# Performance work log

Hardware: AMD Instinct MI355X
Metric: run time of the kernel (lower is better)

The kernel has to match this reference:

```python
import jax, jax.numpy as jnp
import numpy as np
from functools import partial

BN_EPS = 1e-5

def conv2d(x, w, pad):
    # x: [N,C,H,W], w: [O,I,kh,kw]
    return jax.lax.conv_general_dilated(
        x, w, window_strides=(1, 1), padding=((pad, pad), (pad, pad)),
        dimension_numbers=("NCHW", "OIHW", "NCHW"))

def bn_prelu(x, gamma, beta, mean, var, alpha):
    # eval-mode BatchNorm2d followed by single-parameter PReLU
    scale = gamma * jax.lax.rsqrt(var + BN_EPS)
    h = x * scale[None, :, None, None] + (beta - mean * scale)[None, :, None, None]
    return jnp.where(h >= 0, h, alpha * h)

def unfold3x3(x):
    # torch nn.Unfold(3, padding=1): output layout [N, C*9, H*W]
    N, C, H, W = x.shape
    xp = jnp.pad(x, ((0, 0), (0, 0), (1, 1), (1, 1)))
    patches = jnp.stack(
        [xp[:, :, i:i + H, j:j + W] for i in range(3) for j in range(3)],
        axis=2)  # [N, C, 9, H, W] -- row-major identical to [N, C*9, H*W]
    return patches

def setup_inputs() -> dict:
    key = jax.random.key(0)
    ks = jax.random.split(key, 16)
    N, C, H, W = 16, 256, 64, 64
    K2 = 9
    inp = {
        "x": jax.random.normal(ks[0], (N, C, H, W), jnp.float32),
        "y": jax.random.normal(ks[1], (N, C, H, W), jnp.float32),
        # gernerate_kernel_spatial[0]: Conv3x3 C->C + BN + PReLU
        "W1": jax.random.normal(ks[2], (C, C, 3, 3), jnp.float32) * 0.05,
        "g1": jax.random.normal(ks[3], (C,), jnp.float32) * 0.1 + 1.0,
        "b1": jax.random.normal(ks[4], (C,), jnp.float32) * 0.1,
        "m1": jax.random.normal(ks[5], (C,), jnp.float32) * 0.1,
        "v1": jax.random.uniform(ks[6], (C,), jnp.float32, 0.5, 1.5),
        "a1": jnp.float32(0.25),
        # gernerate_kernel_spatial[1]: Conv1x1 C->9 + BN + PReLU
        "W2": jax.random.normal(ks[7], (K2, C, 1, 1), jnp.float32) * 0.05,
        "g2": jax.random.normal(ks[8], (K2,), jnp.float32) * 0.1 + 1.0,
        "b2": jax.random.normal(ks[9], (K2,), jnp.float32) * 0.1,
        "m2": jax.random.normal(ks[10], (K2,), jnp.float32) * 0.1,
        "v2": jax.random.uniform(ks[11], (K2,), jnp.float32, 0.5, 1.5),
        "a2": jnp.float32(0.25),
    }
    return inp

def reference(x, y, W1, g1, b1, m1, v1, a1, W2, g2, b2, m2, v2, a2):
    N, C, H, W = x.shape
    # dynamic per-pixel 3x3 kernel from y: [N, 9, H, W]
    h = bn_prelu(conv2d(y, W1, pad=1), g1, b1, m1, v1, a1)
    kernel = bn_prelu(conv2d(h, W2, pad=0), g2, b2, m2, v2, a2)
    # kernel.reshape(N,9,H,W,1).permute(0,2,3,1,4) -> [N,H,W,9]
    kern = jnp.transpose(kernel, (0, 2, 3, 1))
    # unfold(x) is [N, C*9, H*W]; torch reshapes it ROW-MAJOR to [N,H,W,C,9]
    ux = unfold3x3(x).reshape(N, H, W, C, 9)
    # matmul [N,H,W,C,9] @ [N,H,W,9,1] -> squeeze -> permute to NCHW
    out = jnp.einsum("nhwck,nhwk->nchw", ux, kern)
    return out
```

## Files before the change

kernel.cpp:

```cpp
#include <hip/hip_runtime.h>
#include <hip/hip_bf16.h>

typedef __attribute__((ext_vector_type(8))) short bf16x8;
typedef __attribute__((ext_vector_type(4))) float f32x4;
typedef __attribute__((ext_vector_type(8))) unsigned short u16x8;
typedef __attribute__((ext_vector_type(4))) unsigned short u16x4;

#define BN_EPS 1e-5f

__device__ __forceinline__ unsigned short f2bf(float f) {
  unsigned int u = __float_as_uint(f);
  unsigned int r = u + 0x7FFFu + ((u >> 16) & 1u);
  return (unsigned short)(r >> 16);
}
__device__ __forceinline__ float bf2f(unsigned short u) {
  union { float f; unsigned int i; } v; v.i = ((unsigned int)u) << 16; return v.f;
}

__device__ __forceinline__ void async_ld16(const unsigned short* g, unsigned short* l) {
  __builtin_amdgcn_global_load_lds(
      (const __attribute__((address_space(1))) void*)g,
      (__attribute__((address_space(3))) void*)l, 16, 0, 0);
}

__global__ __launch_bounds__(256) void fold_w1_kernel(
    const float* __restrict__ W1, const float* __restrict__ g1,
    const float* __restrict__ b1, const float* __restrict__ m1,
    const float* __restrict__ v1, const float* __restrict__ W2,
    const float* __restrict__ g2, const float* __restrict__ b2,
    const float* __restrict__ m2, const float* __restrict__ v2,
    unsigned short* __restrict__ Bt, float* __restrict__ bias1,
    float* __restrict__ W2f, float* __restrict__ bias2)
{
  int o = blockIdx.x;
  int t = threadIdx.x;
  if (o == 0) {
    float s1 = g1[t] * rsqrtf(v1[t] + BN_EPS);
    bias1[t] = b1[t] - m1[t] * s1;
    for (int i = t; i < 2304; i += 256) {
      int j = i >> 8;
      float s2 = g2[j] * rsqrtf(v2[j] + BN_EPS);
      W2f[i] = W2[i] * s2;
    }
    if (t < 9) {
      float s2 = g2[t] * rsqrtf(v2[t] + BN_EPS);
      bias2[t] = b2[t] - m2[t] * s2;
    }
  }
  float s = g1[o] * rsqrtf(v1[o] + BN_EPS);
  const float* src = W1 + (size_t)o * 2304 + (size_t)t * 9;
  int chunk = t >> 5, q = (t >> 3) & 3, e = t & 7;
  #pragma unroll
  for (int tap = 0; tap < 9; ++tap) {
    float wv = src[tap] * s;
    int ct = chunk * 9 + tap;
    Bt[(((size_t)ct * 4 + q) * 256 + o) * 8 + e] = f2bf(wv);
  }
}

__global__ __launch_bounds__(256) void transpose_pad_kernel(
    const float* __restrict__ y, unsigned short* __restrict__ yTp)
{
  __shared__ unsigned short T[64][68];
  int t = threadIdx.x;
  int nb = blockIdx.x; int n = nb >> 6, h = nb & 63;
  int w4 = (t & 15) * 4;
  int cl = t >> 4;
  for (int cb = 0; cb < 4; ++cb) {
    __syncthreads();
    #pragma unroll
    for (int r = 0; r < 4; ++r) {
      int c = cb * 64 + cl + r * 16;
      float4 v = *(const float4*)(y + ((((size_t)n * 256 + c) * 64 + h) << 6) + w4);
      u16x4 pv = { f2bf(v.x), f2bf(v.y), f2bf(v.z), f2bf(v.w) };
      *(u16x4*)&T[cl + r * 16][w4] = pv;
    }
    __syncthreads();
    size_t base = ((((size_t)n * 32 + cb * 8) * 66 + (h + 1)) * 66 + 1) * 8;
    #pragma unroll
    for (int pass = 0; pass < 2; ++pass) {
      int w = pass * 32 + (t >> 3);
      int c8 = t & 7;
      u16x8 o;
      #pragma unroll
      for (int i = 0; i < 8; ++i) o[i] = T[c8 * 8 + i][w];
      *(u16x8*)(yTp + base + ((size_t)c8 * (66 * 66) + w) * 8) = o;
    }
  }
  u16x8 z = (u16x8){0, 0, 0, 0, 0, 0, 0, 0};
  size_t nb32 = (size_t)n * 32;
  if (t < 64) {
    int qg = t & 31, side = t >> 5;
    *(u16x8*)(yTp + (((nb32 + qg) * 66 + (h + 1)) * 66 + side * 65) * 8) = z;
  }
  if (h == 0) {
    for (int i = t; i < 2112; i += 256) {
      int qg = i / 66, ww = i - qg * 66;
      *(u16x8*)(yTp + (((nb32 + qg) * 66 + 0) * 66 + ww) * 8) = z;
      *(u16x8*)(yTp + (((nb32 + qg) * 66 + 65) * 66 + ww) * 8) = z;
    }
  }
}

__global__ __launch_bounds__(256, 2) void conv3x3_mfma_kernel(
    const unsigned short* __restrict__ yTp, const unsigned short* __restrict__ Bt,
    const float* __restrict__ bias1, const float* __restrict__ a1p,
    const float* __restrict__ W2f, const float* __restrict__ bias2,
    const float* __restrict__ a2p, float* __restrict__ kernP)
{
  __shared__ union SM {
    struct { unsigned short A[2][4][4][66][8];
             unsigned short B[2][4][256][8]; } m;
    unsigned short h[128][264];
  } sm;
  __shared__ float w2s[2304];

  int tid = threadIdx.x;
  int w = tid >> 6, l = tid & 63;
  int lr = l & 15, quad = l >> 4;
  int wm = w >> 1, wn = w & 1;
  int bm = blockIdx.x;
  int n = bm >> 5, hb = (bm & 31) * 2;

  for (int i = tid; i < 2304; i += 256) w2s[i] = W2f[i];

  f32x4 acc[4][8];
  #pragma unroll
  for (int im = 0; im < 4; ++im)
    #pragma unroll
    for (int in_ = 0; in_ < 8; ++in_)
      acc[im][in_] = (f32x4){0.f, 0.f, 0.f, 0.f};

  const unsigned short* gaP =
      yTp + (((size_t)n * 32 * 66 + (hb + w)) * 66 + l) * 8;
  const unsigned short* gbP = Bt + (size_t)(w * 64 + l) * 8;

  auto stageA = [&](int buf) {
    async_ld16(gaP,          &sm.m.A[buf][0][w][0][0]);
    async_ld16(gaP + 34848,  &sm.m.A[buf][1][w][0][0]);
    async_ld16(gaP + 69696,  &sm.m.A[buf][2][w][0][0]);
    async_ld16(gaP + 104544, &sm.m.A[buf][3][w][0][0]);
    if (l < 2) {
      async_ld16(gaP + 512,          &sm.m.A[buf][0][w][64][0]);
      async_ld16(gaP + 34848 + 512,  &sm.m.A[buf][1][w][64][0]);
      async_ld16(gaP + 69696 + 512,  &sm.m.A[buf][2][w][64][0]);
      async_ld16(gaP + 104544 + 512, &sm.m.A[buf][3][w][64][0]);
    }
    gaP += 139392;
  };
  auto stageB = [&](int buf) {
    async_ld16(gbP,        &sm.m.B[buf][0][w * 64][0]);
    async_ld16(gbP + 2048, &sm.m.B[buf][1][w * 64][0]);
    async_ld16(gbP + 4096, &sm.m.B[buf][2][w * 64][0]);
    async_ld16(gbP + 6144, &sm.m.B[buf][3][w * 64][0]);
    gbP += 8192;
  };

  stageA(0);
  stageB(0);

  int ab = 0, bb = 0;
  #pragma unroll 1
  for (int c = 0; c < 8; ++c) {
    #pragma unroll 1
    for (int t = 0; t < 9; ++t) {
      __syncthreads();
      if (t < 8 || c < 7) stageB(bb ^ 1);
      if (t == 0 && c < 7) stageA(ab ^ 1);

      int ti = t / 3, tj = t - 3 * ti;
      bf16x8 af[4], bfr[8];
      #pragma unroll
      for (int im = 0; im < 4; ++im)
        af[im] = *(const bf16x8*)&sm.m.A[ab][quad][wm + ti][im * 16 + lr + tj][0];
      #pragma unroll
      for (int in_ = 0; in_ < 8; ++in_)
        bfr[in_] = *(const bf16x8*)&sm.m.B[bb][quad][wn * 128 + in_ * 16 + lr][0];
      #pragma unroll
      for (int im = 0; im < 4; ++im)
        #pragma unroll
        for (int in_ = 0; in_ < 8; ++in_)
          acc[im][in_] = __builtin_amdgcn_mfma_f32_16x16x32_bf16(
              af[im], bfr[in_], acc[im][in_], 0, 0, 0);

      bb ^= 1;
    }
    ab ^= 1;
  }

  __syncthreads();

  float a1 = a1p[0];
  #pragma unroll
  for (int in_ = 0; in_ < 8; ++in_) {
    int cch = wn * 128 + in_ * 16 + lr;
    float bs = bias1[cch];
    #pragma unroll
    for (int im = 0; im < 4; ++im) {
      int p0 = wm * 64 + im * 16 + quad * 4;
      #pragma unroll
      for (int r = 0; r < 4; ++r) {
        float v = acc[im][in_][r] + bs;
        v = (v >= 0.f) ? v : a1 * v;
        sm.h[p0 + r][cch] = f2bf(v);
      }
    }
  }
  __syncthreads();

  float a2 = a2p[0];
  int seg = tid & 3, pr = tid >> 2;
  float b2r[9];
  #pragma unroll
  for (int j = 0; j < 9; ++j) b2r[j] = bias2[j];
  #pragma unroll
  for (int rd = 0; rd < 2; ++rd) {
    int pl = rd * 64 + pr;
    float acc2[9];
    #pragma unroll
    for (int j = 0; j < 9; ++j) acc2[j] = 0.f;
    #pragma unroll
    for (int k = 0; k < 8; ++k) {
      int c0 = seg * 8 + k * 32;
      u16x8 hv = *(const u16x8*)&sm.h[pl][c0];
      float hf[8];
      #pragma unroll
      for (int i = 0; i < 8; ++i) hf[i] = bf2f(hv[i]);
      #pragma unroll
      for (int j = 0; j < 9; ++j)
        #pragma unroll
        for (int i = 0; i < 8; ++i)
          acc2[j] = fmaf(hf[i], w2s[j * 256 + c0 + i], acc2[j]);
    }
    #pragma unroll
    for (int j = 0; j < 9; ++j) {
      acc2[j] += __shfl_xor(acc2[j], 1);
      acc2[j] += __shfl_xor(acc2[j], 2);
    }
    if (seg == 0) {
      size_t gp = (size_t)bm * 128 + pl;
      #pragma unroll
      for (int j = 0; j < 9; ++j) {
        float v = acc2[j] + b2r[j];
        v = (v >= 0.f) ? v : a2 * v;
        kernP[j * 65536 + gp] = v;
      }
    }
  }
}

__global__ __launch_bounds__(256) void apply_dyn_kernel(
    const float* __restrict__ x, const float* __restrict__ kernP,
    float* __restrict__ out)
{
  __shared__ float xs[66 * 67];
  __shared__ float ks[9][16];
  int t = threadIdx.x;
  int b = blockIdx.x;
  int g = b & 3;
  int nh = b >> 2;
  int n = nh >> 6, hp = nh & 63;
  int c = 4 * hp + g;

  const float* xplane = x + (((size_t)n * 256 + c) << 12);
  for (int i = t; i < 1024; i += 256) {
    float4 v = *(const float4*)(xplane + i * 4);
    int row = i >> 4;
    int col = (i & 15) * 4;
    float* d = &xs[(row + 1) * 67 + col + 1];
    d[0] = v.x; d[1] = v.y; d[2] = v.z; d[3] = v.w;
  }
  if (t < 67) { xs[t] = 0.f; xs[65 * 67 + t] = 0.f; }
  if (t < 128) { int r = (t >> 1) + 1; int cc = (t & 1) * 65; xs[r * 67 + cc] = 0.f; }
  int pbase = n * 4096 + hp * 64 + g * 16;
  for (int i = t; i < 144; i += 256)
    ks[i / 16][i & 15] = kernP[(i / 16) * 65536 + pbase + (i & 15)];
  __syncthreads();

  int s = t & 15;
  int crow = t >> 4;
  float ksr[9];
  #pragma unroll
  for (int k2 = 0; k2 < 9; ++k2) ksr[k2] = ks[k2][s];

  int r0 = s * 2304 + crow * 144;
  int k0 = r0 >> 12;
  int rem0 = r0 & 4095;
  int wcol = rem0 & 63;
  int ti0 = (k0 >= 6) ? 2 : ((k0 >= 3) ? 1 : 0);
  int tj0 = k0 - 3 * ti0;
  int addr = (rem0 >> 6) * 67 + wcol + ti0 * 67 + tj0;
  int cnt = 4096 - rem0;
  int kN = k0 + 1;
  int tiN = (kN >= 6) ? 2 : ((kN >= 3) ? 1 : 0);
  int addrAtCross = tiN * 67 + (kN - 3 * tiN);

  size_t outIdx = (((size_t)n * 256 + crow * 16) << 12) + (hp << 6) + g * 16 + s;
  #pragma unroll 4
  for (int oi = 0; oi < 16; ++oi) {
    float acc = 0.f;
    #pragma unroll
    for (int k2 = 0; k2 < 9; ++k2) {
      acc = fmaf(xs[addr], ksr[k2], acc);
      ++wcol; ++addr;
      if (wcol == 64) { wcol = 0; addr += 3; }
      if (--cnt == 0) addr = addrAtCross;
    }
    out[outIdx + ((size_t)oi << 12)] = acc;
  }
}

extern "C" void kernel_launch(void* const* d_in, const int* in_sizes, int n_in,
                              void* d_out, int out_size, void* d_ws, size_t ws_size,
                              hipStream_t stream) {
  const float* x  = (const float*)d_in[0];
  const float* y  = (const float*)d_in[1];
  const float* W1 = (const float*)d_in[2];
  const float* g1 = (const float*)d_in[3];
  const float* b1 = (const float*)d_in[4];
  const float* m1 = (const float*)d_in[5];
  const float* v1 = (const float*)d_in[6];
  const float* a1 = (const float*)d_in[7];
  const float* W2 = (const float*)d_in[8];
  const float* g2 = (const float*)d_in[9];
  const float* b2 = (const float*)d_in[10];
  const float* m2 = (const float*)d_in[11];
  const float* v2 = (const float*)d_in[12];
  const float* a2 = (const float*)d_in[13];
  float* out = (float*)d_out;

  char* ws = (char*)d_ws;
  size_t off = 0;
  const size_t yTp_bytes = (size_t)16 * 66 * 66 * 256 * 2;
  unsigned short* yTp = (unsigned short*)(ws + off); off += yTp_bytes;
  unsigned short* Bt  = (unsigned short*)(ws + off); off += (size_t)589824 * 2;
  float* kernP = (float*)(ws + off); off += (size_t)589824 * 4;
  float* bias1 = (float*)(ws + off); off += 1024;
  float* W2f   = (float*)(ws + off); off += 9216;
  float* bias2 = (float*)(ws + off); off += 64;

  fold_w1_kernel<<<256, 256, 0, stream>>>(W1, g1, b1, m1, v1, W2, g2, b2, m2, v2,
                                          Bt, bias1, W2f, bias2);
  transpose_pad_kernel<<<1024, 256, 0, stream>>>(y, yTp);
  conv3x3_mfma_kernel<<<512, 256, 0, stream>>>(yTp, Bt, bias1, a1,
                                               W2f, bias2, a2, kernP);
  apply_dyn_kernel<<<4096, 256, 0, stream>>>(x, kernP, out);
}
```

Before: 313.3 us.

## Load conv weights directly to registers with double buffering, drop LDS B staging

Weight (B) fragments are no longer staged through LDS with async loads. Each lane now reads its 8 bf16x8 fragments straight from global memory into registers, with two register buffers in a software pipeline, and a __syncthreads is issued only once per 9 taps when the A tile is swapped. This cuts LDS traffic and LDS footprint and removes eight of every nine block barriers. In exchange it uses more VGPRs for the second B buffer under launch_bounds(256,2), and it duplicates global or L2 reads of B across waves, since waves sharing wn load the same data.

```diff
diff --git a/kernel.cpp b/kernel.cpp
--- a/kernel.cpp
+++ b/kernel.cpp
@@ -109,8 +109,7 @@
     const float* __restrict__ a2p, float* __restrict__ kernP)
 {
   __shared__ union SM {
-    struct { unsigned short A[2][4][4][66][8];
-             unsigned short B[2][4][256][8]; } m;
+    unsigned short A[2][4][4][66][8];
     unsigned short h[128][264];
   } sm;
   __shared__ float w2s[2304];
@@ -133,59 +132,64 @@
 
   const unsigned short* gaP =
       yTp + (((size_t)n * 32 * 66 + (hb + w)) * 66 + l) * 8;
-  const unsigned short* gbP = Bt + (size_t)(w * 64 + l) * 8;
-
   auto stageA = [&](int buf) {
-    async_ld16(gaP,          &sm.m.A[buf][0][w][0][0]);
-    async_ld16(gaP + 34848,  &sm.m.A[buf][1][w][0][0]);
-    async_ld16(gaP + 69696,  &sm.m.A[buf][2][w][0][0]);
-    async_ld16(gaP + 104544, &sm.m.A[buf][3][w][0][0]);
+    async_ld16(gaP,          &sm.A[buf][0][w][0][0]);
+    async_ld16(gaP + 34848,  &sm.A[buf][1][w][0][0]);
+    async_ld16(gaP + 69696,  &sm.A[buf][2][w][0][0]);
+    async_ld16(gaP + 104544, &sm.A[buf][3][w][0][0]);
     if (l < 2) {
-      async_ld16(gaP + 512,          &sm.m.A[buf][0][w][64][0]);
-      async_ld16(gaP + 34848 + 512,  &sm.m.A[buf][1][w][64][0]);
-      async_ld16(gaP + 69696 + 512,  &sm.m.A[buf][2][w][64][0]);
-      async_ld16(gaP + 104544 + 512, &sm.m.A[buf][3][w][64][0]);
+      async_ld16(gaP + 512,          &sm.A[buf][0][w][64][0]);
+      async_ld16(gaP + 34848 + 512,  &sm.A[buf][1][w][64][0]);
+      async_ld16(gaP + 69696 + 512,  &sm.A[buf][2][w][64][0]);
+      async_ld16(gaP + 104544 + 512, &sm.A[buf][3][w][64][0]);
     }
     gaP += 139392;
   };
-  auto stageB = [&](int buf) {
-    async_ld16(gbP,        &sm.m.B[buf][0][w * 64][0]);
-    async_ld16(gbP + 2048, &sm.m.B[buf][1][w * 64][0]);
-    async_ld16(gbP + 4096, &sm.m.B[buf][2][w * 64][0]);
-    async_ld16(gbP + 6144, &sm.m.B[buf][3][w * 64][0]);
-    gbP += 8192;
+
+  const unsigned short* gbBase = Bt + (size_t)(quad * 256 + wn * 128 + lr) * 8;
+  auto loadB = [&](bf16x8* dst, int tt) {
+    const unsigned short* p = gbBase + ((size_t)tt << 13);
+    #pragma unroll
+    for (int in_ = 0; in_ < 8; ++in_)
+      dst[in_] = *(const bf16x8*)(p + in_ * 128);
   };
 
+  auto computeTap = [&](const bf16x8* b, int ab, int tap) {
+    int ti = (tap >= 6) ? 2 : ((tap >= 3) ? 1 : 0);
+    int tj = tap - 3 * ti;
+    bf16x8 af[4];
+    #pragma unroll
+    for (int im = 0; im < 4; ++im)
+      af[im] = *(const bf16x8*)&sm.A[ab][quad][wm + ti][im * 16 + lr + tj][0];
+    #pragma unroll
+    for (int im = 0; im < 4; ++im)
+      #pragma unroll
+      for (int in_ = 0; in_ < 8; ++in_)
+        acc[im][in_] = __builtin_amdgcn_mfma_f32_16x16x32_bf16(
+            af[im], b[in_], acc[im][in_], 0, 0, 0);
+  };
+
   stageA(0);
-  stageB(0);
-
-  int ab = 0, bb = 0;
+  bf16x8 bA[8], bB[8];
+  loadB(bA, 0);
+
+  int tap = 0, ab = 0;
   #pragma unroll 1
-  for (int c = 0; c < 8; ++c) {
-    #pragma unroll 1
-    for (int t = 0; t < 9; ++t) {
+  for (int tt = 0; tt < 72; tt += 2) {
+    if (tap == 0) {
       __syncthreads();
-      if (t < 8 || c < 7) stageB(bb ^ 1);
-      if (t == 0 && c < 7) stageA(ab ^ 1);
-
-      int ti = t / 3, tj = t - 3 * ti;
-      bf16x8 af[4], bfr[8];
-      #pragma unroll
-      for (int im = 0; im < 4; ++im)
-        af[im] = *(const bf16x8*)&sm.m.A[ab][quad][wm + ti][im * 16 + lr + tj][0];
-      #pragma unroll
-      for (int in_ = 0; in_ < 8; ++in_)
-        bfr[in_] = *(const bf16x8*)&sm.m.B[bb][quad][wn * 128 + in_ * 16 + lr][0];
-      #pragma unroll
-      for (int im = 0; im < 4; ++im)
-        #pragma unroll
-        for (int in_ = 0; in_ < 8; ++in_)
-          acc[im][in_] = __builtin_amdgcn_mfma_f32_16x16x32_bf16(
-              af[im], bfr[in_], acc[im][in_], 0, 0, 0);
-
-      bb ^= 1;
-    }
-    ab ^= 1;
+      if (tt < 63) stageA(ab ^ 1);
+    }
+    loadB(bB, tt + 1);
+    computeTap(bA, ab, tap);
+    if (++tap == 9) { tap = 0; ab ^= 1; }
+    if (tap == 0) {
+      __syncthreads();
+      if (tt + 1 < 63) stageA(ab ^ 1);
+    }
+    if (tt + 2 < 72) loadB(bA, tt + 2);
+    computeTap(bB, ab, tap);
+    if (++tap == 9) { tap = 0; ab ^= 1; }
   }
 
   __syncthreads();
```

Result: no change. 307.3 us (-1.9%).
